# Performance work log

Measured on AMD Instinct MI355X. Metric: run time of the kernel, lower is better.

## Reference

```python
import jax, jax.numpy as jnp
import numpy as np

SYNC_COST = 10.0
T_START_MS, T_END_MS = 0, 500
EPS = 1e-7
_bs = np.logspace(-3, 0, 20)
BIN_MS = [int(np.round(b * 1000)) for b in _bs[_bs < (0.5 - 0.0) / 2]]  # 16 static bin widths in ms


def setup_inputs() -> dict:
    key = jax.random.key(0)
    k1, k2 = jax.random.split(key, 2)
    n_trials, T_total, n_neurons = 8, 600, 30000
    n_e, n_samples, max_count = 25000, 50, 200
    spikes = (jax.random.uniform(k1, (n_trials, T_total, n_neurons)) < 0.02).astype(jnp.float32)
    experimental_fanos_mean = jax.random.uniform(k2, (len(BIN_MS),), jnp.float32) * 2.0 + 0.5
    rng = np.random.default_rng(0)
    sample_trials = jnp.asarray(rng.integers(0, n_trials, n_samples), jnp.int32)
    # counts ~ clip(N(70,30), 15, max_count), as in the original sampling logic
    counts = np.clip(rng.normal(70, 30, n_samples).astype(np.int64), 15, max_count)
    sample_ids = jnp.asarray(rng.integers(0, n_e, (n_samples, max_count)), jnp.int64)
    sample_mask = jnp.asarray(np.arange(max_count)[None, :] < counts[:, None], jnp.float32)
    return {"spikes": spikes, "experimental_fanos_mean": experimental_fanos_mean,
            "sample_trials": sample_trials, "sample_ids": sample_ids, "sample_mask": sample_mask}


def _pop_fano(x):
    # x: [T, S] population spike-count time series per sample
    T = x.shape[0]
    fanos = []
    for bs in BIN_MS:  # static, small loop over 16 bin widths
        nb = T // bs
        counts = x[: nb * bs].reshape(nb, bs, -1).sum(axis=1)  # [nb, S]
        mean = jnp.maximum(counts.mean(axis=0), EPS)
        fanos.append(jnp.var(counts, axis=0) / mean)  # ddof=0, like tf.math.reduce_variance
    return jnp.stack(fanos)  # [n_bins, S]


def reference(spikes, experimental_fanos_mean, sample_trials, sample_ids, sample_mask):
    sp = spikes[:, T_START_MS:T_END_MS, :]  # [n_trials, T, N]

    def gather_sum(trial, ids, m):
        g = jnp.take(jnp.take(sp, trial, axis=0), ids, axis=1)  # [T, C]
        return jnp.sum(g * m[None, :], axis=-1)                 # [T]

    sel = jax.vmap(gather_sum)(sample_trials, sample_ids, sample_mask)  # [S, T]
    fanos = _pop_fano(sel.T)          # [n_bins, S]
    fanos_mean = fanos.mean(axis=1)   # [n_bins]
    mse = jnp.mean(jnp.square(experimental_fanos_mean - fanos_mean))
    return SYNC_COST * mse
```

## Files before the change

### kernel.cpp

```cpp
#include <hip/hip_runtime.h>
#include <hip/hip_bf16.h>

#define N_TRIALS   8
#define T_TOTAL    600
#define N_NEURONS  30000
#define NEED_N     25000
#define T_USE      500
#define N_SAMPLES  50
#define MAX_COUNT  200
#define N_BINS     16
#define GROUPS     98
#define WPR        (GROUPS * 4)
#define ITERS      25
#define EPS_D      1e-7

__device__ __constant__ int BIN_SIZES[N_BINS] = {1,1,2,3,4,6,9,13,18,26,38,55,78,113,162,234};

__global__ __launch_bounds__(256) void cnt_kernel(
    const float* __restrict__ mask, int* __restrict__ cnts)
{
    int w    = (blockIdx.x * 256 + threadIdx.x) >> 6;
    int lane = threadIdx.x & 63;
    if (w >= N_SAMPLES) return;
    const float* m = mask + w * MAX_COUNT;
    float sum = 0.f;
    for (int j = lane; j < MAX_COUNT; j += 64) sum += m[j];
    for (int k = 32; k; k >>= 1) sum += __shfl_xor(sum, k);
    if (lane == 0) cnts[w] = (int)(sum + 0.5f);
}

__global__ __launch_bounds__(256) void row_kernel(
    const float* __restrict__ spikes,
    const int*   __restrict__ trials,
    const int*   __restrict__ ids,
    const int*   __restrict__ cnts,
    float*       __restrict__ sel)
{
    __shared__ unsigned long long bm[WPR];
    int tid  = threadIdx.x;
    int wv   = tid >> 6;
    int lane = tid & 63;
    int r    = blockIdx.x;
    int tr   = r / T_USE;
    int t    = r % T_USE;
    const float* row = spikes + ((size_t)tr * T_TOTAL + t) * N_NEURONS;

    for (int i = 0; i < ITERS; ++i) {
        int n0 = i * 1024 + tid * 4;
        float4 v = make_float4(0.f, 0.f, 0.f, 0.f);
        if (n0 < NEED_N)
            v = *reinterpret_cast<const float4*>(row + n0);
        unsigned long long b0 = __ballot(v.x != 0.f);
        unsigned long long b1 = __ballot(v.y != 0.f);
        unsigned long long b2 = __ballot(v.z != 0.f);
        unsigned long long b3 = __ballot(v.w != 0.f);
        int g = i * 4 + wv;
        if (g < GROUPS && lane == 0) {
            bm[g*4+0] = b0; bm[g*4+1] = b1; bm[g*4+2] = b2; bm[g*4+3] = b3;
        }
    }
    __syncthreads();

    for (int s = wv; s < N_SAMPLES; s += 4) {
        if (trials[s] != tr) continue;
        int cnt = cnts[s];
        const int* sid = ids + s * MAX_COUNT;
        int c = 0;
        for (int base = 0; base < MAX_COUNT; base += 64) {
            int j = base + lane;
            bool pred = false;
            if (j < cnt) {
                int n = sid[j];
                unsigned long long w = bm[((n >> 8) << 2) | (n & 3)];
                pred = (w >> ((n >> 2) & 63)) & 1ull;
            }
            c += __popcll(__ballot(pred));
        }
        if (lane == 0) sel[s * T_USE + t] = (float)c;
    }
}

__global__ __launch_bounds__(256) void fano_stage(
    const float* __restrict__ sel,
    float*       __restrict__ fano)
{
    int w    = (blockIdx.x * 256 + threadIdx.x) >> 6;
    int lane = threadIdx.x & 63;
    if (w >= N_BINS * N_SAMPLES) return;
    int bin = w / N_SAMPLES;
    int s   = w % N_SAMPLES;
    int bs  = BIN_SIZES[bin];
    int nb  = T_USE / bs;
    const float* rowp = sel + s * T_USE;

    double sum = 0.0, sumsq = 0.0;
    for (int b = lane; b < nb; b += 64) {
        double c = 0.0;
        int base = b * bs;
        for (int q = 0; q < bs; ++q) c += (double)rowp[base + q];
        sum   += c;
        sumsq += c * c;
    }
    for (int k = 32; k; k >>= 1) {
        sum   += __shfl_xor(sum,   k);
        sumsq += __shfl_xor(sumsq, k);
    }
    if (lane == 0) {
        double mean = sum / nb;
        double var  = sumsq / nb - mean * mean;
        double m2   = mean < EPS_D ? EPS_D : mean;
        fano[w] = (float)(var / m2);
    }
}

__global__ void final_kernel(
    const float* __restrict__ fano,
    const float* __restrict__ expf,
    float*       __restrict__ out)
{
    int tid = threadIdx.x;
    double d2 = 0.0;
    if (tid < N_BINS) {
        double acc = 0.0;
        for (int s = 0; s < N_SAMPLES; ++s) acc += (double)fano[tid * N_SAMPLES + s];
        double fm   = acc / N_SAMPLES;
        double diff = (double)expf[tid] - fm;
        d2 = diff * diff;
    }
    for (int k = 32; k; k >>= 1) d2 += __shfl_xor(d2, k);
    if (tid == 0) out[0] = (float)(10.0 * d2 / N_BINS);
}

extern "C" void kernel_launch(void* const* d_in, const int* in_sizes, int n_in,
                              void* d_out, int out_size, void* d_ws, size_t ws_size,
                              hipStream_t stream)
{
    const float* spikes = (const float*)d_in[0];
    const float* expf   = (const float*)d_in[1];
    const int*   trials = (const int*)d_in[2];
    const int*   ids    = (const int*)d_in[3];
    const float* mask   = (const float*)d_in[4];
    float* out = (float*)d_out;

    float* sel  = (float*)d_ws;
    float* fano = sel + N_SAMPLES * T_USE;
    int*   cnts = (int*)(fano + N_BINS * N_SAMPLES);

    cnt_kernel<<<(N_SAMPLES * 64 + 255) / 256, 256, 0, stream>>>(mask, cnts);

    row_kernel<<<N_TRIALS * T_USE, 256, 0, stream>>>(spikes, trials, ids, cnts, sel);

    fano_stage<<<(N_BINS * N_SAMPLES * 64 + 255) / 256, 256, 0, stream>>>(sel, fano);

    final_kernel<<<1, 64, 0, stream>>>(fano, expf, out);
}
```

Measured before the change: 727.6 us.

## Split row bitmask compression and sample probing into separate kernels

The fused per-row kernel is replaced by a fully parallel compress kernel, one thread per float4 quad, which writes per-row spike bitmasks to a global workspace. A probe kernel, one block per time step, then loads the bitmasks for all eight trials into shared memory and counts selected neurons for every sample. This raises memory-level parallelism on the dominant spike read and removes the per-block loop and barrier. The cost is an extra kernel launch and a bitmask round trip through global memory.

```diff
diff --git a/kernel.cpp b/kernel.cpp
--- a/kernel.cpp
+++ b/kernel.cpp
@@ -1,5 +1,7 @@
 #include <hip/hip_runtime.h>
 #include <hip/hip_bf16.h>
+
+typedef unsigned long long ull;
 
 #define N_TRIALS   8
 #define T_TOTAL    600
@@ -11,7 +13,9 @@
 #define N_BINS     16
 #define GROUPS     98
 #define WPR        (GROUPS * 4)
-#define ITERS      25
+#define QPR        (GROUPS * 64)
+#define N_ROWS     (N_TRIALS * T_USE)
+#define TOT_QUADS  (N_ROWS * QPR)
 #define EPS_D      1e-7
 
 __device__ __constant__ int BIN_SIZES[N_BINS] = {1,1,2,3,4,6,9,13,18,26,38,55,78,113,162,234};
@@ -29,40 +33,53 @@
     if (lane == 0) cnts[w] = (int)(sum + 0.5f);
 }
 
-__global__ __launch_bounds__(256) void row_kernel(
-    const float* __restrict__ spikes,
-    const int*   __restrict__ trials,
-    const int*   __restrict__ ids,
-    const int*   __restrict__ cnts,
-    float*       __restrict__ sel)
+__global__ __launch_bounds__(256) void compress_kernel(
+    const float* __restrict__ spikes, ull* __restrict__ bm)
 {
-    __shared__ unsigned long long bm[WPR];
+    unsigned u = blockIdx.x * 256 + threadIdx.x;
+    unsigned q = u % QPR;
+    unsigned r = u / QPR;
+    unsigned tr = r / T_USE;
+    unsigned rowg = r + tr * (T_TOTAL - T_USE);
+
+    float4 v = make_float4(0.f, 0.f, 0.f, 0.f);
+    if (q < NEED_N / 4)
+        v = *reinterpret_cast<const float4*>(spikes + (size_t)rowg * N_NEURONS + q * 4);
+
+    ull b0 = __ballot(v.x != 0.f);
+    ull b1 = __ballot(v.y != 0.f);
+    ull b2 = __ballot(v.z != 0.f);
+    ull b3 = __ballot(v.w != 0.f);
+
+    if ((threadIdx.x & 63) == 0) {
+        ull* dst = bm + (size_t)r * WPR + (q >> 6) * 4;
+        ulonglong2 p0; p0.x = b0; p0.y = b1;
+        ulonglong2 p1; p1.x = b2; p1.y = b3;
+        *reinterpret_cast<ulonglong2*>(dst)     = p0;
+        *reinterpret_cast<ulonglong2*>(dst + 2) = p1;
+    }
+}
+
+__global__ __launch_bounds__(256) void probe_kernel(
+    const ull* __restrict__ bm,
+    const int* __restrict__ trials,
+    const int* __restrict__ ids,
+    const int* __restrict__ cnts,
+    float*     __restrict__ sel)
+{
+    __shared__ ull lbm[N_TRIALS][WPR];
+    int t    = blockIdx.x;
     int tid  = threadIdx.x;
     int wv   = tid >> 6;
     int lane = tid & 63;
-    int r    = blockIdx.x;
-    int tr   = r / T_USE;
-    int t    = r % T_USE;
-    const float* row = spikes + ((size_t)tr * T_TOTAL + t) * N_NEURONS;
 
-    for (int i = 0; i < ITERS; ++i) {
-        int n0 = i * 1024 + tid * 4;
-        float4 v = make_float4(0.f, 0.f, 0.f, 0.f);
-        if (n0 < NEED_N)
-            v = *reinterpret_cast<const float4*>(row + n0);
-        unsigned long long b0 = __ballot(v.x != 0.f);
-        unsigned long long b1 = __ballot(v.y != 0.f);
-        unsigned long long b2 = __ballot(v.z != 0.f);
-        unsigned long long b3 = __ballot(v.w != 0.f);
-        int g = i * 4 + wv;
-        if (g < GROUPS && lane == 0) {
-            bm[g*4+0] = b0; bm[g*4+1] = b1; bm[g*4+2] = b2; bm[g*4+3] = b3;
-        }
-    }
+    for (int tr = 0; tr < N_TRIALS; ++tr)
+        for (int j = tid; j < WPR; j += 256)
+            lbm[tr][j] = bm[(size_t)(tr * T_USE + t) * WPR + j];
     __syncthreads();
 
     for (int s = wv; s < N_SAMPLES; s += 4) {
-        if (trials[s] != tr) continue;
+        int tr  = trials[s];
         int cnt = cnts[s];
         const int* sid = ids + s * MAX_COUNT;
         int c = 0;
@@ -71,7 +88,7 @@
             bool pred = false;
             if (j < cnt) {
                 int n = sid[j];
-                unsigned long long w = bm[((n >> 8) << 2) | (n & 3)];
+                ull w = lbm[tr][((n >> 8) << 2) | (n & 3)];
                 pred = (w >> ((n >> 2) & 63)) & 1ull;
             }
             c += __popcll(__ballot(pred));
@@ -142,13 +159,16 @@
     const float* mask   = (const float*)d_in[4];
     float* out = (float*)d_out;
 
-    float* sel  = (float*)d_ws;
+    ull*   bm   = (ull*)d_ws;
+    float* sel  = (float*)(bm + (size_t)N_ROWS * WPR);
     float* fano = sel + N_SAMPLES * T_USE;
     int*   cnts = (int*)(fano + N_BINS * N_SAMPLES);
 
     cnt_kernel<<<(N_SAMPLES * 64 + 255) / 256, 256, 0, stream>>>(mask, cnts);
 
-    row_kernel<<<N_TRIALS * T_USE, 256, 0, stream>>>(spikes, trials, ids, cnts, sel);
+    compress_kernel<<<TOT_QUADS / 256, 256, 0, stream>>>(spikes, bm);
+
+    probe_kernel<<<T_USE, 256, 0, stream>>>(bm, trials, ids, cnts, sel);
 
     fano_stage<<<(N_BINS * N_SAMPLES * 64 + 255) / 256, 256, 0, stream>>>(sel, fano);
 
```

Measured after the change: 725.1 us. Within noise of the previous version (-0.4%).
